# Kernel tuning notes

Measured on AMD Instinct MI355X. Metric: run time of the kernel, lower is better.

## Reference

```python
import jax, jax.numpy as jnp
import numpy as np

N = 50000      # nodes
E = 800000     # edges (avg degree 16)
D = 3          # dim_world
L = 128        # latent_dim
STEPS = 10     # message passing steps
RID = 64       # num_rigid_ids
REMB = 16      # rigid_embedding_dim


def _mlp2(x, w1, b1, w2, b2):
    # 2-layer MLP: Linear -> ReLU -> Linear (layer_norm=False, dropout=0)
    return jnp.maximum(x @ w1 + b1, 0.0) @ w2 + b2


def setup_inputs() -> dict:
    key = jax.random.key(0)
    ks = jax.random.split(key, 24)
    f32 = jnp.float32

    def lin(k, i, o):
        return (jax.random.normal(k, (i, o), f32) / np.sqrt(i)).astype(f32)

    node_in = 2 * D + 1 + REMB   # 23
    edge_in = 2 * D + 2 + 1      # 9

    receivers = jax.random.randint(ks[4], (E,), 0, N)
    # no self edges (radius_graph uses include_self_edges=False)
    senders = (receivers + jax.random.randint(ks[3], (E,), 1, N)) % N

    inp = {
        'positions': jax.random.uniform(ks[0], (N, D), f32),
        'velocities': jax.random.normal(ks[1], (N, D), f32),
        'rigid_id': jax.random.randint(ks[2], (N,), 0, RID),
        'senders': senders,
        'receivers': receivers,
        'rigid_emb': jax.random.normal(ks[5], (RID, REMB), f32) * 0.1,
        # node encoder
        'ne_w1': lin(ks[6], node_in, L), 'ne_b1': jnp.zeros((L,), f32),
        'ne_w2': lin(ks[7], L, L),       'ne_b2': jnp.zeros((L,), f32),
        # edge encoder
        'ee_w1': lin(ks[8], edge_in, L), 'ee_b1': jnp.zeros((L,), f32),
        'ee_w2': lin(ks[9], L, L),       'ee_b2': jnp.zeros((L,), f32),
        # processor blocks (stacked over STEPS)
        'pe_w1': (jax.random.normal(ks[10], (STEPS, 3 * L, L), f32) / np.sqrt(3 * L)).astype(f32),
        'pe_b1': jnp.zeros((STEPS, L), f32),
        'pe_w2': (jax.random.normal(ks[11], (STEPS, L, L), f32) / np.sqrt(L)).astype(f32),
        'pe_b2': jnp.zeros((STEPS, L), f32),
        'pn_w1': (jax.random.normal(ks[12], (STEPS, 2 * L, L), f32) / np.sqrt(2 * L)).astype(f32),
        'pn_b1': jnp.zeros((STEPS, L), f32),
        'pn_w2': (jax.random.normal(ks[13], (STEPS, L, L), f32) / np.sqrt(L)).astype(f32),
        'pn_b2': jnp.zeros((STEPS, L), f32),
        # decoder (2 layers -> output_dim = D)
        'de_w1': lin(ks[14], L, L), 'de_b1': jnp.zeros((L,), f32),
        'de_w2': lin(ks[15], L, D), 'de_b2': jnp.zeros((D,), f32),
    }
    return inp


def reference(positions, velocities, rigid_id, senders, receivers, rigid_emb,
              ne_w1, ne_b1, ne_w2, ne_b2, ee_w1, ee_b1, ee_w2, ee_b2,
              pe_w1, pe_b1, pe_w2, pe_b2, pn_w1, pn_b1, pn_w2, pn_b2,
              de_w1, de_b1, de_w2, de_b2):
    n = positions.shape[0]
    dt = positions.dtype

    # ----- feature construction (build_gns_graph_inputs + rigid features) -----
    deg = jax.ops.segment_sum(jnp.ones(receivers.shape, dt), receivers, num_segments=n)[:, None]
    center = positions.mean(axis=0, keepdims=True)
    rigid_feat = rigid_emb[rigid_id]                                # [N, REMB]
    node_feat = jnp.concatenate([velocities, positions - center, deg, rigid_feat], axis=-1)

    rel_pos = positions[senders] - positions[receivers]             # [E, D]
    rel_vel = velocities[senders] - velocities[receivers]
    sq = jnp.sum(rel_pos * rel_pos, axis=-1, keepdims=True)
    dist = jnp.sqrt(sq)
    same = (rigid_id[senders] == rigid_id[receivers]).astype(dt)[:, None]
    edge_feat = jnp.concatenate([rel_pos, rel_vel, dist, sq, same], axis=-1)

    # ----- encode -----
    nl = _mlp2(node_feat, ne_w1, ne_b1, ne_w2, ne_b2)               # [N, L]
    el = _mlp2(edge_feat, ee_w1, ee_b1, ee_w2, ee_b2)               # [E, L]

    # ----- process: gather -> edge MLP -> scatter-add -> node MLP, residual -----
    for i in range(pe_w1.shape[0]):
        edge_in = jnp.concatenate([el, nl[senders], nl[receivers]], axis=-1)  # [E, 3L]
        el = el + _mlp2(edge_in, pe_w1[i], pe_b1[i], pe_w2[i], pe_b2[i])
        agg = jax.ops.segment_sum(el, receivers, num_segments=n)              # [N, L]
        node_in = jnp.concatenate([nl, agg], axis=-1)                         # [N, 2L]
        nl = nl + _mlp2(node_in, pn_w1[i], pn_b1[i], pn_w2[i], pn_b2[i])

    # ----- decode -----
    return _mlp2(nl, de_w1, de_b1, de_w2, de_b2)                    # [N, D]
```

## Files before the change

### kernel.cpp

```cpp
#include <hip/hip_runtime.h>
#include <hip/hip_bf16.h>

#define NN 50000
#define NE 800000
#define LDIM 128
#define NSTEPS 10

typedef __hip_bfloat16 bf16;
typedef __bf16 bf8v __attribute__((ext_vector_type(8)));
typedef float f4v __attribute__((ext_vector_type(4)));
typedef unsigned short u16x8 __attribute__((ext_vector_type(8)));

__device__ inline float bflo(unsigned int u) {
    union { unsigned int i; float f; } x; x.i = u << 16; return x.f;
}
__device__ inline float bfhi(unsigned int u) {
    union { unsigned int i; float f; } x; x.i = u & 0xffff0000u; return x.f;
}
__device__ inline unsigned short f2bf(float f) {
    __hip_bfloat16 h = __float2bfloat16(f);
    unsigned short u; __builtin_memcpy(&u, &h, 2); return u;
}


__global__ void k_hist(const int* __restrict__ rcv, int* __restrict__ cnt) {
    int i = blockIdx.x * 256 + threadIdx.x;
    if (i < NE) atomicAdd(&cnt[rcv[i]], 1);
}

__global__ __launch_bounds__(1024) void k_scan(
    const int* __restrict__ cnt, int* __restrict__ row_start,
    int* __restrict__ cur, float* __restrict__ degf) {
    __shared__ int part[1024];
    const int t = threadIdx.x;
    const int CH = (NN + 1023) / 1024;
    int b0 = t * CH, b1 = b0 + CH; if (b1 > NN) b1 = NN; if (b0 > NN) b0 = NN;
    int s = 0;
    for (int i = b0; i < b1; i++) s += cnt[i];
    part[t] = s;
    __syncthreads();
    for (int off = 1; off < 1024; off <<= 1) {
        int v = (t >= off) ? part[t - off] : 0;
        __syncthreads();
        part[t] += v;
        __syncthreads();
    }
    int run = part[t] - s;
    for (int i = b0; i < b1; i++) {
        row_start[i] = run; cur[i] = run; degf[i] = (float)cnt[i];
        run += cnt[i];
    }
    if (t == 1023) row_start[NN] = part[1023];
}

__global__ void k_scatter(const int* __restrict__ snd, const int* __restrict__ rcv,
                          int* __restrict__ cur,
                          unsigned short* __restrict__ snd_p, unsigned short* __restrict__ rcv_p) {
    int i = blockIdx.x * 256 + threadIdx.x;
    if (i < NE) {
        int r = rcv[i];
        int p = atomicAdd(&cur[r], 1);
        snd_p[p] = (unsigned short)snd[i];
        rcv_p[p] = (unsigned short)r;
    }
}

__global__ void k_center(const float* __restrict__ pos, float* __restrict__ csum) {
    __shared__ float s[3][256];
    float a = 0.f, b = 0.f, c = 0.f;
    for (int i = blockIdx.x * 256 + threadIdx.x; i < NN; i += gridDim.x * 256) {
        a += pos[3 * i]; b += pos[3 * i + 1]; c += pos[3 * i + 2];
    }
    int t = threadIdx.x;
    s[0][t] = a; s[1][t] = b; s[2][t] = c;
    __syncthreads();
    for (int off = 128; off > 0; off >>= 1) {
        if (t < off) {
            s[0][t] += s[0][t + off];
            s[1][t] += s[1][t + off];
            s[2][t] += s[2][t + off];
        }
        __syncthreads();
    }
    if (t == 0) {
        atomicAdd(&csum[0], s[0][0]);
        atomicAdd(&csum[1], s[1][0]);
        atomicAdd(&csum[2], s[2][0]);
    }
}


__global__ void k_prep_w(const float* __restrict__ w, unsigned short* __restrict__ wf,
                         int KT, int Ksrc, int lo) {
    int b = blockIdx.x;
    int s = b / (KT * 8), rem = b % (KT * 8);
    int kt = rem / 8, nt = rem % 8;
    int lane = threadIdx.x, col = lane & 15, quad = lane >> 4;
    const float* W = w + (size_t)s * Ksrc * 128;
    u16x8 o;
#pragma unroll
    for (int jj = 0; jj < 8; jj++) {
        int k = kt * 32 + quad * 8 + jj;
        float x = (k < Ksrc) ? W[(size_t)k * 128 + nt * 16 + col] : 0.f;
        unsigned short h = f2bf(x);
        if (lo) h = f2bf(x - bflo(h));
        o[jj] = h;
    }
    *(u16x8*)(wf + (((size_t)b) * 64 + lane) * 8) = o;
}


__global__ __launch_bounds__(256) void k_agg(
    const unsigned short* __restrict__ el, const int* __restrict__ row_start,
    unsigned short* __restrict__ agg) {
    const int wave = threadIdx.x >> 6, lane = threadIdx.x & 63;
    const int n = blockIdx.x * 4 + wave;
    if (n >= NN) return;
    const int sub = lane >> 4, c16 = lane & 15;
    const int st = row_start[n], en = row_start[n + 1];
    float s[8];
#pragma unroll
    for (int k = 0; k < 8; k++) s[k] = 0.f;
    for (int q = st + sub; q < en; q += 4) {
        uint4 v = *(const uint4*)(el + (size_t)q * 128 + c16 * 8);
        s[0] += bflo(v.x); s[1] += bfhi(v.x);
        s[2] += bflo(v.y); s[3] += bfhi(v.y);
        s[4] += bflo(v.z); s[5] += bfhi(v.z);
        s[6] += bflo(v.w); s[7] += bfhi(v.w);
    }
#pragma unroll
    for (int k = 0; k < 8; k++) {
        s[k] += __shfl_xor(s[k], 16);
        s[k] += __shfl_xor(s[k], 32);
    }
    if (sub == 0) {
        u16x8 o;
#pragma unroll
        for (int k = 0; k < 8; k++) o[k] = f2bf(s[k]);
        *(u16x8*)(agg + (size_t)n * 128 + c16 * 8) = o;
    }
}


__global__ __launch_bounds__(256) void k_node_enc_m(
    const float* __restrict__ pos, const float* __restrict__ vel,
    const int* __restrict__ rid, const float* __restrict__ remb,
    const float* __restrict__ degf, const float* __restrict__ csum,
    const unsigned short* __restrict__ w1h, const unsigned short* __restrict__ w1l,
    const float* __restrict__ b1,
    const unsigned short* __restrict__ w2h, const unsigned short* __restrict__ w2l,
    const float* __restrict__ b2,
    unsigned short* __restrict__ nlh, unsigned short* __restrict__ nll) {
    __shared__ __align__(16) unsigned short feat_s[32 * 72];
    __shared__ __align__(16) unsigned short hid_s[32 * 264];
    const int tid = threadIdx.x, wave = tid >> 6, lane = tid & 63;
    const int col = lane & 15, quad = lane >> 4;
    bf8v W1H[2], W1L[2], W2H[4][2], W2L[4][2];
#pragma unroll
    for (int t = 0; t < 2; t++) {
        W1H[t] = *(const bf8v*)(w1h + ((size_t)(2 * wave + t) * 64 + lane) * 8);
        W1L[t] = *(const bf8v*)(w1l + ((size_t)(2 * wave + t) * 64 + lane) * 8);
    }
#pragma unroll
    for (int kt = 0; kt < 4; kt++)
#pragma unroll
        for (int t = 0; t < 2; t++) {
            W2H[kt][t] = *(const bf8v*)(w2h + ((size_t)(kt * 8 + 2 * wave + t) * 64 + lane) * 8);
            W2L[kt][t] = *(const bf8v*)(w2l + ((size_t)(kt * 8 + 2 * wave + t) * 64 + lane) * 8);
        }
    float bias1[2], bias2[2];
#pragma unroll
    for (int t = 0; t < 2; t++) {
        bias1[t] = b1[(2 * wave + t) * 16 + col];
        bias2[t] = b2[(2 * wave + t) * 16 + col];
    }
    float cx = csum[0] * (1.0f / NN), cy = csum[1] * (1.0f / NN), cz = csum[2] * (1.0f / NN);
    uint4 z = {0u, 0u, 0u, 0u};
    for (int s2 = tid; s2 < 288; s2 += 256) *(uint4*)(feat_s + s2 * 8) = z;

    for (int it = 0; it < 4; it++) {
        const int base = blockIdx.x * 128 + it * 32;
        if (base >= NN) break;
        __syncthreads();
        if (tid < 32) {
            int n = base + tid; if (n > NN - 1) n = NN - 1;
            float v[23];
            v[0] = vel[3 * n]; v[1] = vel[3 * n + 1]; v[2] = vel[3 * n + 2];
            v[3] = pos[3 * n] - cx; v[4] = pos[3 * n + 1] - cy; v[5] = pos[3 * n + 2] - cz;
            v[6] = degf[n];
            int rb = rid[n] * 16;
#pragma unroll
            for (int k = 0; k < 16; k++) v[7 + k] = remb[rb + k];
            unsigned short* f = feat_s + tid * 72;
#pragma unroll
            for (int k = 0; k < 23; k++) {
                unsigned short h = f2bf(v[k]);
                f[k] = h; f[32 + k] = f2bf(v[k] - bflo(h));
            }
        }
        __syncthreads();
        f4v acc[2][2];
#pragma unroll
        for (int mt = 0; mt < 2; mt++)
#pragma unroll
            for (int t = 0; t < 2; t++) acc[mt][t] = (f4v){0.f, 0.f, 0.f, 0.f};
        {
            bf8v a0h = *(const bf8v*)(feat_s + col * 72 + quad * 8);
            bf8v a1h = *(const bf8v*)(feat_s + (16 + col) * 72 + quad * 8);
            bf8v a0l = *(const bf8v*)(feat_s + col * 72 + 32 + quad * 8);
            bf8v a1l = *(const bf8v*)(feat_s + (16 + col) * 72 + 32 + quad * 8);
#pragma unroll
            for (int t = 0; t < 2; t++) {
                acc[0][t] = __builtin_amdgcn_mfma_f32_16x16x32_bf16(a0h, W1H[t], acc[0][t], 0, 0, 0);
                acc[1][t] = __builtin_amdgcn_mfma_f32_16x16x32_bf16(a1h, W1H[t], acc[1][t], 0, 0, 0);
                acc[0][t] = __builtin_amdgcn_mfma_f32_16x16x32_bf16(a0l, W1H[t], acc[0][t], 0, 0, 0);
                acc[1][t] = __builtin_amdgcn_mfma_f32_16x16x32_bf16(a1l, W1H[t], acc[1][t], 0, 0, 0);
                acc[0][t] = __builtin_amdgcn_mfma_f32_16x16x32_bf16(a0h, W1L[t], acc[0][t], 0, 0, 0);
                acc[1][t] = __builtin_amdgcn_mfma_f32_16x16x32_bf16(a1h, W1L[t], acc[1][t], 0, 0, 0);
            }
        }
#pragma unroll
        for (int mt = 0; mt < 2; mt++)
#pragma unroll
            for (int t = 0; t < 2; t++) {
                const int nc = (2 * wave + t) * 16 + col;
#pragma unroll
                for (int r = 0; r < 4; r++) {
                    float h = fmaxf(acc[mt][t][r] + bias1[t], 0.f);
                    unsigned short hh = f2bf(h);
                    hid_s[(mt * 16 + quad * 4 + r) * 264 + nc] = hh;
                    hid_s[(mt * 16 + quad * 4 + r) * 264 + 128 + nc] = f2bf(h - bflo(hh));
                }
            }
        __syncthreads();
#pragma unroll
        for (int mt = 0; mt < 2; mt++)
#pragma unroll
            for (int t = 0; t < 2; t++) acc[mt][t] = (f4v){0.f, 0.f, 0.f, 0.f};
#pragma unroll
        for (int kt = 0; kt < 8; kt++) {
            int w = kt & 3;
            bf8v a0 = *(const bf8v*)(hid_s + col * 264 + kt * 32 + quad * 8);
            bf8v a1 = *(const bf8v*)(hid_s + (16 + col) * 264 + kt * 32 + quad * 8);
#pragma unroll
            for (int t = 0; t < 2; t++) {
                acc[0][t] = __builtin_amdgcn_mfma_f32_16x16x32_bf16(a0, W2H[w][t], acc[0][t], 0, 0, 0);
                acc[1][t] = __builtin_amdgcn_mfma_f32_16x16x32_bf16(a1, W2H[w][t], acc[1][t], 0, 0, 0);
            }
        }
#pragma unroll
        for (int kt = 0; kt < 4; kt++) {
            bf8v a0 = *(const bf8v*)(hid_s + col * 264 + kt * 32 + quad * 8);
            bf8v a1 = *(const bf8v*)(hid_s + (16 + col) * 264 + kt * 32 + quad * 8);
#pragma unroll
            for (int t = 0; t < 2; t++) {
                acc[0][t] = __builtin_amdgcn_mfma_f32_16x16x32_bf16(a0, W2L[kt][t], acc[0][t], 0, 0, 0);
                acc[1][t] = __builtin_amdgcn_mfma_f32_16x16x32_bf16(a1, W2L[kt][t], acc[1][t], 0, 0, 0);
            }
        }
        __syncthreads();
#pragma unroll
        for (int mt = 0; mt < 2; mt++)
#pragma unroll
            for (int t = 0; t < 2; t++) {
                const int nc = (2 * wave + t) * 16 + col;
#pragma unroll
                for (int r = 0; r < 4; r++) {
                    const int row = mt * 16 + quad * 4 + r;
                    float v = acc[mt][t][r] + bias2[t];
                    unsigned short hh = f2bf(v);
                    hid_s[row * 264 + nc] = hh;
                    hid_s[row * 264 + 128 + nc] = f2bf(v - bflo(hh));
                }
            }
        __syncthreads();
#pragma unroll
        for (int p = 0; p < 2; p++) {
            int s2 = p * 256 + tid, e = s2 >> 4, c16 = s2 & 15;
            if (base + e < NN) {
                *(uint4*)(nlh + (size_t)(base + e) * 128 + c16 * 8) =
                    *(const uint4*)(hid_s + e * 264 + c16 * 8);
                *(uint4*)(nll + (size_t)(base + e) * 128 + c16 * 8) =
                    *(const uint4*)(hid_s + e * 264 + 128 + c16 * 8);
            }
        }
    }
}


__global__ __launch_bounds__(256) void k_edge_enc_m(
    const float* __restrict__ pos, const float* __restrict__ vel,
    const int* __restrict__ rid,
    const unsigned short* __restrict__ snd, const unsigned short* __restrict__ rcv,
    const unsigned short* __restrict__ w1h, const unsigned short* __restrict__ w1l,
    const float* __restrict__ b1,
    const unsigned short* __restrict__ w2h, const unsigned short* __restrict__ w2l,
    const float* __restrict__ b2,
    unsigned short* __restrict__ el) {
    __shared__ __align__(16) unsigned short feat_s[32 * 72];
    __shared__ __align__(16) unsigned short hid_s[32 * 264];
    const int tid = threadIdx.x, wave = tid >> 6, lane = tid & 63;
    const int col = lane & 15, quad = lane >> 4;
    bf8v W1H[2], W1L[2], W2H[4][2], W2L[4][2];
#pragma unroll
    for (int t = 0; t < 2; t++) {
        W1H[t] = *(const bf8v*)(w1h + ((size_t)(2 * wave + t) * 64 + lane) * 8);
        W1L[t] = *(const bf8v*)(w1l + ((size_t)(2 * wave + t) * 64 + lane) * 8);
    }
#pragma unroll
    for (int kt = 0; kt < 4; kt++)
#pragma unroll
        for (int t = 0; t < 2; t++) {
            W2H[kt][t] = *(const bf8v*)(w2h + ((size_t)(kt * 8 + 2 * wave + t) * 64 + lane) * 8);
            W2L[kt][t] = *(const bf8v*)(w2l + ((size_t)(kt * 8 + 2 * wave + t) * 64 + lane) * 8);
        }
    float bias1[2], bias2[2];
#pragma unroll
    for (int t = 0; t < 2; t++) {
        bias1[t] = b1[(2 * wave + t) * 16 + col];
        bias2[t] = b2[(2 * wave + t) * 16 + col];
    }
    uint4 z = {0u, 0u, 0u, 0u};
    for (int s2 = tid; s2 < 288; s2 += 256) *(uint4*)(feat_s + s2 * 8) = z;

    for (int it = 0; it < 4; it++) {
        const int base = blockIdx.x * 128 + it * 32;
        __syncthreads();
        if (tid < 32) {
            int e = base + tid;
            int s = snd[e], r = rcv[e];
            float v[9];
            v[0] = pos[3 * s] - pos[3 * r]; v[1] = pos[3 * s + 1] - pos[3 * r + 1]; v[2] = pos[3 * s + 2] - pos[3 * r + 2];
            v[3] = vel[3 * s] - vel[3 * r]; v[4] = vel[3 * s + 1] - vel[3 * r + 1]; v[5] = vel[3 * s + 2] - vel[3 * r + 2];
            float sq = v[0] * v[0] + v[1] * v[1] + v[2] * v[2];
            v[6] = sqrtf(sq); v[7] = sq;
            v[8] = (rid[s] == rid[r]) ? 1.f : 0.f;
            unsigned short* f = feat_s + tid * 72;
#pragma unroll
            for (int k = 0; k < 9; k++) {
                unsigned short h = f2bf(v[k]);
                f[k] = h; f[32 + k] = f2bf(v[k] - bflo(h));
            }
        }
        __syncthreads();
        f4v acc[2][2];
#pragma unroll
        for (int mt = 0; mt < 2; mt++)
#pragma unroll
            for (int t = 0; t < 2; t++) acc[mt][t] = (f4v){0.f, 0.f, 0.f, 0.f};
        {
            bf8v a0h = *(const bf8v*)(feat_s + col * 72 + quad * 8);
            bf8v a1h = *(const bf8v*)(feat_s + (16 + col) * 72 + quad * 8);
            bf8v a0l = *(const bf8v*)(feat_s + col * 72 + 32 + quad * 8);
            bf8v a1l = *(const bf8v*)(feat_s + (16 + col) * 72 + 32 + quad * 8);
#pragma unroll
            for (int t = 0; t < 2; t++) {
                acc[0][t] = __builtin_amdgcn_mfma_f32_16x16x32_bf16(a0h, W1H[t], acc[0][t], 0, 0, 0);
                acc[1][t] = __builtin_amdgcn_mfma_f32_16x16x32_bf16(a1h, W1H[t], acc[1][t], 0, 0, 0);
                acc[0][t] = __builtin_amdgcn_mfma_f32_16x16x32_bf16(a0l, W1H[t], acc[0][t], 0, 0, 0);
                acc[1][t] = __builtin_amdgcn_mfma_f32_16x16x32_bf16(a1l, W1H[t], acc[1][t], 0, 0, 0);
                acc[0][t] = __builtin_amdgcn_mfma_f32_16x16x32_bf16(a0h, W1L[t], acc[0][t], 0, 0, 0);
                acc[1][t] = __builtin_amdgcn_mfma_f32_16x16x32_bf16(a1h, W1L[t], acc[1][t], 0, 0, 0);
            }
        }
#pragma unroll
        for (int mt = 0; mt < 2; mt++)
#pragma unroll
            for (int t = 0; t < 2; t++) {
                const int nc = (2 * wave + t) * 16 + col;
#pragma unroll
                for (int r = 0; r < 4; r++) {
                    float h = fmaxf(acc[mt][t][r] + bias1[t], 0.f);
                    unsigned short hh = f2bf(h);
                    hid_s[(mt * 16 + quad * 4 + r) * 264 + nc] = hh;
                    hid_s[(mt * 16 + quad * 4 + r) * 264 + 128 + nc] = f2bf(h - bflo(hh));
                }
            }
        __syncthreads();
#pragma unroll
        for (int mt = 0; mt < 2; mt++)
#pragma unroll
            for (int t = 0; t < 2; t++) acc[mt][t] = (f4v){0.f, 0.f, 0.f, 0.f};
#pragma unroll
        for (int kt = 0; kt < 8; kt++) {
            int w = kt & 3;
            bf8v a0 = *(const bf8v*)(hid_s + col * 264 + kt * 32 + quad * 8);
            bf8v a1 = *(const bf8v*)(hid_s + (16 + col) * 264 + kt * 32 + quad * 8);
#pragma unroll
            for (int t = 0; t < 2; t++) {
                acc[0][t] = __builtin_amdgcn_mfma_f32_16x16x32_bf16(a0, W2H[w][t], acc[0][t], 0, 0, 0);
                acc[1][t] = __builtin_amdgcn_mfma_f32_16x16x32_bf16(a1, W2H[w][t], acc[1][t], 0, 0, 0);
            }
        }
#pragma unroll
        for (int kt = 0; kt < 4; kt++) {
            bf8v a0 = *(const bf8v*)(hid_s + col * 264 + kt * 32 + quad * 8);
            bf8v a1 = *(const bf8v*)(hid_s + (16 + col) * 264 + kt * 32 + quad * 8);
#pragma unroll
            for (int t = 0; t < 2; t++) {
                acc[0][t] = __builtin_amdgcn_mfma_f32_16x16x32_bf16(a0, W2L[kt][t], acc[0][t], 0, 0, 0);
                acc[1][t] = __builtin_amdgcn_mfma_f32_16x16x32_bf16(a1, W2L[kt][t], acc[1][t], 0, 0, 0);
            }
        }
        __syncthreads();
#pragma unroll
        for (int mt = 0; mt < 2; mt++)
#pragma unroll
            for (int t = 0; t < 2; t++) {
                const int nc = (2 * wave + t) * 16 + col;
#pragma unroll
                for (int r = 0; r < 4; r++)
                    hid_s[(mt * 16 + quad * 4 + r) * 264 + nc] = f2bf(acc[mt][t][r] + bias2[t]);
            }
        __syncthreads();
#pragma unroll
        for (int p = 0; p < 2; p++) {
            int s2 = p * 256 + tid, e = s2 >> 4, c16 = s2 & 15;
            *(uint4*)(el + (size_t)(base + e) * 128 + c16 * 8) =
                *(const uint4*)(hid_s + e * 264 + c16 * 8);
        }
    }
}


__global__ __launch_bounds__(256) void k_edge_step(
    unsigned short* __restrict__ el, const unsigned short* __restrict__ nlh,
    const unsigned short* __restrict__ snd, const unsigned short* __restrict__ rcv,
    const unsigned short* __restrict__ w1f, const float* __restrict__ b1,
    const unsigned short* __restrict__ w2f, const float* __restrict__ b2) {
    __shared__ __align__(16) unsigned short inl_s[32 * 392];
    __shared__ __align__(16) unsigned short hid_s[32 * 136];
    const int tid = threadIdx.x;
    const int wave = tid >> 6, lane = tid & 63;
    const int col = lane & 15, quad = lane >> 4;
    const int erow = tid >> 4, c16 = tid & 15;

    bf8v W1[12][2], W2[4][2];
#pragma unroll
    for (int kt = 0; kt < 12; kt++)
#pragma unroll
        for (int t = 0; t < 2; t++)
            W1[kt][t] = *(const bf8v*)(w1f + ((size_t)(kt * 8 + 2 * wave + t) * 64 + lane) * 8);
#pragma unroll
    for (int kt = 0; kt < 4; kt++)
#pragma unroll
        for (int t = 0; t < 2; t++)
            W2[kt][t] = *(const bf8v*)(w2f + ((size_t)(kt * 8 + 2 * wave + t) * 64 + lane) * 8);
    float bias1[2], bias2[2];
#pragma unroll
    for (int t = 0; t < 2; t++) {
        bias1[t] = b1[(2 * wave + t) * 16 + col];
        bias2[t] = b2[(2 * wave + t) * 16 + col];
    }

    uint4 pf_s[2];
#pragma unroll
    for (int p = 0; p < 2; p++) {
        int ge = blockIdx.x * 128 + p * 16 + erow;
        pf_s[p] = *(const uint4*)(nlh + (size_t)snd[ge] * 128 + c16 * 8);
    }

    for (int it = 0; it < 4; it++) {
        const int base = blockIdx.x * 128 + it * 32;
        __syncthreads();
#pragma unroll
        for (int p = 0; p < 2; p++) {
            int e = p * 16 + erow;
            int ge = base + e;
            *(uint4*)(inl_s + e * 392 + c16 * 8) =
                *(const uint4*)(el + (size_t)ge * 128 + c16 * 8);
            *(uint4*)(inl_s + e * 392 + 128 + c16 * 8) = pf_s[p];
            *(uint4*)(inl_s + e * 392 + 256 + c16 * 8) =
                *(const uint4*)(nlh + (size_t)rcv[ge] * 128 + c16 * 8);
        }
        if (it < 3) {
#pragma unroll
            for (int p = 0; p < 2; p++) {
                int ge = base + 32 + p * 16 + erow;
                pf_s[p] = *(const uint4*)(nlh + (size_t)snd[ge] * 128 + c16 * 8);
            }
        }
        __syncthreads();

        f4v acc[2][2];
#pragma unroll
        for (int mt = 0; mt < 2; mt++)
#pragma unroll
            for (int t = 0; t < 2; t++) acc[mt][t] = (f4v){0.f, 0.f, 0.f, 0.f};
#pragma unroll
        for (int kt = 0; kt < 12; kt++) {
            bf8v a0 = *(const bf8v*)(inl_s + col * 392 + kt * 32 + quad * 8);
            bf8v a1 = *(const bf8v*)(inl_s + (16 + col) * 392 + kt * 32 + quad * 8);
            acc[0][0] = __builtin_amdgcn_mfma_f32_16x16x32_bf16(a0, W1[kt][0], acc[0][0], 0, 0, 0);
            acc[0][1] = __builtin_amdgcn_mfma_f32_16x16x32_bf16(a0, W1[kt][1], acc[0][1], 0, 0, 0);
            acc[1][0] = __builtin_amdgcn_mfma_f32_16x16x32_bf16(a1, W1[kt][0], acc[1][0], 0, 0, 0);
            acc[1][1] = __builtin_amdgcn_mfma_f32_16x16x32_bf16(a1, W1[kt][1], acc[1][1], 0, 0, 0);
        }
#pragma unroll
        for (int mt = 0; mt < 2; mt++)
#pragma unroll
            for (int t = 0; t < 2; t++) {
                const int nc = (2 * wave + t) * 16 + col;
#pragma unroll
                for (int r = 0; r < 4; r++) {
                    float v = fmaxf(acc[mt][t][r] + bias1[t], 0.f);
                    hid_s[(mt * 16 + quad * 4 + r) * 136 + nc] = f2bf(v);
                }
            }
        __syncthreads();

#pragma unroll
        for (int mt = 0; mt < 2; mt++)
#pragma unroll
            for (int t = 0; t < 2; t++) acc[mt][t] = (f4v){0.f, 0.f, 0.f, 0.f};
#pragma unroll
        for (int kt = 0; kt < 4; kt++) {
            bf8v a0 = *(const bf8v*)(hid_s + col * 136 + kt * 32 + quad * 8);
            bf8v a1 = *(const bf8v*)(hid_s + (16 + col) * 136 + kt * 32 + quad * 8);
            acc[0][0] = __builtin_amdgcn_mfma_f32_16x16x32_bf16(a0, W2[kt][0], acc[0][0], 0, 0, 0);
            acc[0][1] = __builtin_amdgcn_mfma_f32_16x16x32_bf16(a0, W2[kt][1], acc[0][1], 0, 0, 0);
            acc[1][0] = __builtin_amdgcn_mfma_f32_16x16x32_bf16(a1, W2[kt][0], acc[1][0], 0, 0, 0);
            acc[1][1] = __builtin_amdgcn_mfma_f32_16x16x32_bf16(a1, W2[kt][1], acc[1][1], 0, 0, 0);
        }
        __syncthreads();
#pragma unroll
        for (int mt = 0; mt < 2; mt++)
#pragma unroll
            for (int t = 0; t < 2; t++) {
                const int nc = (2 * wave + t) * 16 + col;
#pragma unroll
                for (int r = 0; r < 4; r++) {
                    const int row = mt * 16 + quad * 4 + r;
                    float v = acc[mt][t][r] + bias2[t] + bflo((unsigned int)inl_s[row * 392 + nc]);
                    hid_s[row * 136 + nc] = f2bf(v);
                }
            }
        __syncthreads();
#pragma unroll
        for (int p = 0; p < 2; p++) {
            int e = p * 16 + erow;
            *(uint4*)(el + (size_t)(base + e) * 128 + c16 * 8) =
                *(const uint4*)(hid_s + e * 136 + c16 * 8);
        }
    }
}


__global__ __launch_bounds__(256) void k_node_step_s(
    unsigned short* __restrict__ nlh, unsigned short* __restrict__ nll,
    const unsigned short* __restrict__ agg,
    const unsigned short* __restrict__ w1h, const unsigned short* __restrict__ w1l,
    const float* __restrict__ b1,
    const unsigned short* __restrict__ w2h, const unsigned short* __restrict__ w2l,
    const float* __restrict__ b2) {
    __shared__ __align__(16) unsigned short a_s[32 * 392];
    __shared__ __align__(16) unsigned short hid_s[32 * 264];
    const int tid = threadIdx.x, wave = tid >> 6, lane = tid & 63;
    const int col = lane & 15, quad = lane >> 4;
    bf8v W1H[8][2], W1L[8][2], W2H[4][2], W2L[4][2];
#pragma unroll
    for (int kt = 0; kt < 8; kt++)
#pragma unroll
        for (int t = 0; t < 2; t++) {
            W1H[kt][t] = *(const bf8v*)(w1h + ((size_t)(kt * 8 + 2 * wave + t) * 64 + lane) * 8);
            W1L[kt][t] = *(const bf8v*)(w1l + ((size_t)(kt * 8 + 2 * wave + t) * 64 + lane) * 8);
        }
#pragma unroll
    for (int kt = 0; kt < 4; kt++)
#pragma unroll
        for (int t = 0; t < 2; t++) {
            W2H[kt][t] = *(const bf8v*)(w2h + ((size_t)(kt * 8 + 2 * wave + t) * 64 + lane) * 8);
            W2L[kt][t] = *(const bf8v*)(w2l + ((size_t)(kt * 8 + 2 * wave + t) * 64 + lane) * 8);
        }
    float bias1[2], bias2[2];
#pragma unroll
    for (int t = 0; t < 2; t++) {
        bias1[t] = b1[(2 * wave + t) * 16 + col];
        bias2[t] = b2[(2 * wave + t) * 16 + col];
    }
    for (int it = 0; it < 2; it++) {
        const int base = blockIdx.x * 64 + it * 32;
        if (base >= NN) break;
        __syncthreads();
#pragma unroll
        for (int p = 0; p < 2; p++) {
            int e = p * 16 + (tid >> 4), c16 = tid & 15;
            int n = base + e; if (n > NN - 1) n = NN - 1;
            *(uint4*)(a_s + e * 392 + c16 * 8) =
                *(const uint4*)(nlh + (size_t)n * 128 + c16 * 8);
            *(uint4*)(a_s + e * 392 + 128 + c16 * 8) =
                *(const uint4*)(nll + (size_t)n * 128 + c16 * 8);
            *(uint4*)(a_s + e * 392 + 256 + c16 * 8) =
                *(const uint4*)(agg + (size_t)n * 128 + c16 * 8);
        }
        __syncthreads();

        f4v acc[2][2];
#pragma unroll
        for (int mt = 0; mt < 2; mt++)
#pragma unroll
            for (int t = 0; t < 2; t++) acc[mt][t] = (f4v){0.f, 0.f, 0.f, 0.f};
#pragma unroll
        for (int kt = 0; kt < 8; kt++) {
            bf8v a0 = *(const bf8v*)(a_s + col * 392 + kt * 32 + quad * 8);
            bf8v a1 = *(const bf8v*)(a_s + (16 + col) * 392 + kt * 32 + quad * 8);
#pragma unroll
            for (int t = 0; t < 2; t++) {
                acc[0][t] = __builtin_amdgcn_mfma_f32_16x16x32_bf16(a0, W1H[kt & 3][t], acc[0][t], 0, 0, 0);
                acc[1][t] = __builtin_amdgcn_mfma_f32_16x16x32_bf16(a1, W1H[kt & 3][t], acc[1][t], 0, 0, 0);
            }
        }
#pragma unroll
        for (int kt = 0; kt < 4; kt++) {
            bf8v a0 = *(const bf8v*)(a_s + col * 392 + 256 + kt * 32 + quad * 8);
            bf8v a1 = *(const bf8v*)(a_s + (16 + col) * 392 + 256 + kt * 32 + quad * 8);
#pragma unroll
            for (int t = 0; t < 2; t++) {
                acc[0][t] = __builtin_amdgcn_mfma_f32_16x16x32_bf16(a0, W1H[4 + kt][t], acc[0][t], 0, 0, 0);
                acc[1][t] = __builtin_amdgcn_mfma_f32_16x16x32_bf16(a1, W1H[4 + kt][t], acc[1][t], 0, 0, 0);
            }
        }
#pragma unroll
        for (int kt = 0; kt < 4; kt++) {
            bf8v a0 = *(const bf8v*)(a_s + col * 392 + kt * 32 + quad * 8);
            bf8v a1 = *(const bf8v*)(a_s + (16 + col) * 392 + kt * 32 + quad * 8);
#pragma unroll
            for (int t = 0; t < 2; t++) {
                acc[0][t] = __builtin_amdgcn_mfma_f32_16x16x32_bf16(a0, W1L[kt][t], acc[0][t], 0, 0, 0);
                acc[1][t] = __builtin_amdgcn_mfma_f32_16x16x32_bf16(a1, W1L[kt][t], acc[1][t], 0, 0, 0);
            }
        }
#pragma unroll
        for (int kt = 0; kt < 4; kt++) {
            bf8v a0 = *(const bf8v*)(a_s + col * 392 + 256 + kt * 32 + quad * 8);
            bf8v a1 = *(const bf8v*)(a_s + (16 + col) * 392 + 256 + kt * 32 + quad * 8);
#pragma unroll
            for (int t = 0; t < 2; t++) {
                acc[0][t] = __builtin_amdgcn_mfma_f32_16x16x32_bf16(a0, W1L[4 + kt][t], acc[0][t], 0, 0, 0);
                acc[1][t] = __builtin_amdgcn_mfma_f32_16x16x32_bf16(a1, W1L[4 + kt][t], acc[1][t], 0, 0, 0);
            }
        }
#pragma unroll
        for (int mt = 0; mt < 2; mt++)
#pragma unroll
            for (int t = 0; t < 2; t++) {
                const int nc = (2 * wave + t) * 16 + col;
#pragma unroll
                for (int r = 0; r < 4; r++) {
                    float h = fmaxf(acc[mt][t][r] + bias1[t], 0.f);
                    unsigned short hh = f2bf(h);
                    hid_s[(mt * 16 + quad * 4 + r) * 264 + nc] = hh;
                    hid_s[(mt * 16 + quad * 4 + r) * 264 + 128 + nc] = f2bf(h - bflo(hh));
                }
            }
        __syncthreads();
#pragma unroll
        for (int mt = 0; mt < 2; mt++)
#pragma unroll
            for (int t = 0; t < 2; t++) acc[mt][t] = (f4v){0.f, 0.f, 0.f, 0.f};
#pragma unroll
        for (int kt = 0; kt < 8; kt++) {
            int w = kt & 3;
            bf8v a0 = *(const bf8v*)(hid_s + col * 264 + kt * 32 + quad * 8);
            bf8v a1 = *(const bf8v*)(hid_s + (16 + col) * 264 + kt * 32 + quad * 8);
#pragma unroll
            for (int t = 0; t < 2; t++) {
                acc[0][t] = __builtin_amdgcn_mfma_f32_16x16x32_bf16(a0, W2H[w][t], acc[0][t], 0, 0, 0);
                acc[1][t] = __builtin_amdgcn_mfma_f32_16x16x32_bf16(a1, W2H[w][t], acc[1][t], 0, 0, 0);
            }
        }
#pragma unroll
        for (int kt = 0; kt < 4; kt++) {
            bf8v a0 = *(const bf8v*)(hid_s + col * 264 + kt * 32 + quad * 8);
            bf8v a1 = *(const bf8v*)(hid_s + (16 + col) * 264 + kt * 32 + quad * 8);
#pragma unroll
            for (int t = 0; t < 2; t++) {
                acc[0][t] = __builtin_amdgcn_mfma_f32_16x16x32_bf16(a0, W2L[kt][t], acc[0][t], 0, 0, 0);
                acc[1][t] = __builtin_amdgcn_mfma_f32_16x16x32_bf16(a1, W2L[kt][t], acc[1][t], 0, 0, 0);
            }
        }
        __syncthreads();
#pragma unroll
        for (int mt = 0; mt < 2; mt++)
#pragma unroll
            for (int t = 0; t < 2; t++) {
                const int nc = (2 * wave + t) * 16 + col;
#pragma unroll
                for (int r = 0; r < 4; r++) {
                    const int row = mt * 16 + quad * 4 + r;
                    float res = bflo((unsigned int)a_s[row * 392 + nc]) +
                                bflo((unsigned int)a_s[row * 392 + 128 + nc]);
                    float v = acc[mt][t][r] + bias2[t] + res;
                    unsigned short hh = f2bf(v);
                    hid_s[row * 264 + nc] = hh;
                    hid_s[row * 264 + 128 + nc] = f2bf(v - bflo(hh));
                }
            }
        __syncthreads();
#pragma unroll
        for (int p = 0; p < 2; p++) {
            int e = p * 16 + (tid >> 4), c16 = tid & 15;
            if (base + e < NN) {
                *(uint4*)(nlh + (size_t)(base + e) * 128 + c16 * 8) =
                    *(const uint4*)(hid_s + e * 264 + c16 * 8);
                *(uint4*)(nll + (size_t)(base + e) * 128 + c16 * 8) =
                    *(const uint4*)(hid_s + e * 264 + 128 + c16 * 8);
            }
        }
    }
}


__global__ __launch_bounds__(128) void k_decode(
    const unsigned short* __restrict__ nlh, const unsigned short* __restrict__ nll,
    const float* __restrict__ w1, const float* __restrict__ b1,
    const float* __restrict__ w2, const float* __restrict__ b2,
    float* __restrict__ out) {
    __shared__ float inl[16][128];
    __shared__ float hid[16][128];
    int j = threadIdx.x;
    int base = blockIdx.x * 16;
    for (int e = 0; e < 16; e++)
        inl[e][j] = bflo((unsigned int)nlh[(size_t)(base + e) * 128 + j]) +
                    bflo((unsigned int)nll[(size_t)(base + e) * 128 + j]);
    __syncthreads();
    float acc[16];
#pragma unroll
    for (int e = 0; e < 16; e++) acc[e] = b1[j];
    for (int kc = 0; kc < 16; kc++) {
        float w[8];
#pragma unroll
        for (int t = 0; t < 8; t++) w[t] = w1[(kc * 8 + t) * 128 + j];
#pragma unroll
        for (int e = 0; e < 16; e++) {
            float4 h0 = *(const float4*)&inl[e][kc * 8];
            float4 h1 = *(const float4*)&inl[e][kc * 8 + 4];
            acc[e] = fmaf(h0.x, w[0], acc[e]); acc[e] = fmaf(h0.y, w[1], acc[e]);
            acc[e] = fmaf(h0.z, w[2], acc[e]); acc[e] = fmaf(h0.w, w[3], acc[e]);
            acc[e] = fmaf(h1.x, w[4], acc[e]); acc[e] = fmaf(h1.y, w[5], acc[e]);
            acc[e] = fmaf(h1.z, w[6], acc[e]); acc[e] = fmaf(h1.w, w[7], acc[e]);
        }
    }
#pragma unroll
    for (int e = 0; e < 16; e++) hid[e][j] = fmaxf(acc[e], 0.f);
    __syncthreads();
    if (j < 48) {
        int e = j / 3, ch = j - 3 * (j / 3);
        float s = b2[ch];
        for (int k = 0; k < 128; k++) s = fmaf(hid[e][k], w2[k * 3 + ch], s);
        out[(size_t)(base + e) * 3 + ch] = s;
    }
}


extern "C" void kernel_launch(void* const* d_in, const int* in_sizes, int n_in,
                              void* d_out, int out_size, void* d_ws, size_t ws_size,
                              hipStream_t stream) {
    (void)in_sizes; (void)n_in; (void)out_size; (void)ws_size;
    const float* pos   = (const float*)d_in[0];
    const float* vel   = (const float*)d_in[1];
    const int*   rid   = (const int*)d_in[2];
    const int*   snd   = (const int*)d_in[3];
    const int*   rcv   = (const int*)d_in[4];
    const float* remb  = (const float*)d_in[5];
    const float* ne_w1 = (const float*)d_in[6];
    const float* ne_b1 = (const float*)d_in[7];
    const float* ne_w2 = (const float*)d_in[8];
    const float* ne_b2 = (const float*)d_in[9];
    const float* ee_w1 = (const float*)d_in[10];
    const float* ee_b1 = (const float*)d_in[11];
    const float* ee_w2 = (const float*)d_in[12];
    const float* ee_b2 = (const float*)d_in[13];
    const float* pe_w1 = (const float*)d_in[14];
    const float* pe_b1 = (const float*)d_in[15];
    const float* pe_w2 = (const float*)d_in[16];
    const float* pe_b2 = (const float*)d_in[17];
    const float* pn_w1 = (const float*)d_in[18];
    const float* pn_b1 = (const float*)d_in[19];
    const float* pn_w2 = (const float*)d_in[20];
    const float* pn_b2 = (const float*)d_in[21];
    const float* de_w1 = (const float*)d_in[22];
    const float* de_b1 = (const float*)d_in[23];
    const float* de_w2 = (const float*)d_in[24];
    const float* de_b2 = (const float*)d_in[25];
    float* out = (float*)d_out;

    char* p = (char*)d_ws;
    auto carve = [&](size_t bytes) { void* q = (void*)p; p += (bytes + 15) & ~(size_t)15; return q; };
    unsigned short* el    = (unsigned short*)carve((size_t)NE * LDIM * 2);
    unsigned short* nlh   = (unsigned short*)carve((size_t)NN * LDIM * 2);
    unsigned short* nll   = (unsigned short*)carve((size_t)NN * LDIM * 2);
    unsigned short* agg   = (unsigned short*)carve((size_t)NN * LDIM * 2);
    unsigned short* w1f_e = (unsigned short*)carve((size_t)NSTEPS * 12 * 8 * 512 * 2);
    unsigned short* w2f_e = (unsigned short*)carve((size_t)NSTEPS * 4 * 8 * 512 * 2);
    unsigned short* w1h_n = (unsigned short*)carve((size_t)NSTEPS * 8 * 8 * 512 * 2);
    unsigned short* w1l_n = (unsigned short*)carve((size_t)NSTEPS * 8 * 8 * 512 * 2);
    unsigned short* w2h_n = (unsigned short*)carve((size_t)NSTEPS * 4 * 8 * 512 * 2);
    unsigned short* w2l_n = (unsigned short*)carve((size_t)NSTEPS * 4 * 8 * 512 * 2);
    unsigned short* eew1h = (unsigned short*)carve((size_t)1 * 8 * 512 * 2);
    unsigned short* eew1l = (unsigned short*)carve((size_t)1 * 8 * 512 * 2);
    unsigned short* eew2h = (unsigned short*)carve((size_t)4 * 8 * 512 * 2);
    unsigned short* eew2l = (unsigned short*)carve((size_t)4 * 8 * 512 * 2);
    unsigned short* new1h = (unsigned short*)carve((size_t)1 * 8 * 512 * 2);
    unsigned short* new1l = (unsigned short*)carve((size_t)1 * 8 * 512 * 2);
    unsigned short* new2h = (unsigned short*)carve((size_t)4 * 8 * 512 * 2);
    unsigned short* new2l = (unsigned short*)carve((size_t)4 * 8 * 512 * 2);
    unsigned short* snd_p = (unsigned short*)carve((size_t)NE * 2);
    unsigned short* rcv_p = (unsigned short*)carve((size_t)NE * 2);
    int*            rs    = (int*)carve((size_t)(NN + 1) * 4);
    int*            cnt   = (int*)carve((size_t)NN * 4);
    int*            cur   = (int*)carve((size_t)NN * 4);
    float*          degf  = (float*)carve((size_t)NN * 4);
    float*          csum  = (float*)carve(16);

    hipMemsetAsync(cnt, 0, (size_t)NN * 4, stream);
    hipMemsetAsync(csum, 0, 16, stream);
    k_hist<<<NE / 256, 256, 0, stream>>>(rcv, cnt);
    k_scan<<<1, 1024, 0, stream>>>(cnt, rs, cur, degf);
    k_center<<<64, 256, 0, stream>>>(pos, csum);
    k_scatter<<<NE / 256, 256, 0, stream>>>(snd, rcv, cur, snd_p, rcv_p);
    k_prep_w<<<NSTEPS * 12 * 8, 64, 0, stream>>>(pe_w1, w1f_e, 12, 384, 0);
    k_prep_w<<<NSTEPS * 4 * 8, 64, 0, stream>>>(pe_w2, w2f_e, 4, 128, 0);
    k_prep_w<<<NSTEPS * 8 * 8, 64, 0, stream>>>(pn_w1, w1h_n, 8, 256, 0);
    k_prep_w<<<NSTEPS * 8 * 8, 64, 0, stream>>>(pn_w1, w1l_n, 8, 256, 1);
    k_prep_w<<<NSTEPS * 4 * 8, 64, 0, stream>>>(pn_w2, w2h_n, 4, 128, 0);
    k_prep_w<<<NSTEPS * 4 * 8, 64, 0, stream>>>(pn_w2, w2l_n, 4, 128, 1);
    k_prep_w<<<8, 64, 0, stream>>>(ee_w1, eew1h, 1, 9, 0);
    k_prep_w<<<8, 64, 0, stream>>>(ee_w1, eew1l, 1, 9, 1);
    k_prep_w<<<4 * 8, 64, 0, stream>>>(ee_w2, eew2h, 4, 128, 0);
    k_prep_w<<<4 * 8, 64, 0, stream>>>(ee_w2, eew2l, 4, 128, 1);
    k_prep_w<<<8, 64, 0, stream>>>(ne_w1, new1h, 1, 23, 0);
    k_prep_w<<<8, 64, 0, stream>>>(ne_w1, new1l, 1, 23, 1);
    k_prep_w<<<4 * 8, 64, 0, stream>>>(ne_w2, new2h, 4, 128, 0);
    k_prep_w<<<4 * 8, 64, 0, stream>>>(ne_w2, new2l, 4, 128, 1);

    k_node_enc_m<<<(NN + 127) / 128, 256, 0, stream>>>(pos, vel, rid, remb, degf, csum,
                                                       new1h, new1l, ne_b1, new2h, new2l, ne_b2, nlh, nll);
    k_edge_enc_m<<<NE / 128, 256, 0, stream>>>(pos, vel, rid, snd_p, rcv_p,
                                               eew1h, eew1l, ee_b1, eew2h, eew2l, ee_b2, el);
    for (int i = 0; i < NSTEPS; i++) {
        k_edge_step<<<NE / 128, 256, 0, stream>>>(el, nlh, snd_p, rcv_p,
            w1f_e + (size_t)i * 12 * 8 * 512, pe_b1 + i * 128,
            w2f_e + (size_t)i * 4 * 8 * 512, pe_b2 + i * 128);
        k_agg<<<(NN + 3) / 4, 256, 0, stream>>>(el, rs, agg);
        k_node_step_s<<<(NN + 63) / 64, 256, 0, stream>>>(nlh, nll, agg,
            w1h_n + (size_t)i * 8 * 8 * 512, w1l_n + (size_t)i * 8 * 8 * 512, pn_b1 + i * 128,
            w2h_n + (size_t)i * 4 * 8 * 512, w2l_n + (size_t)i * 4 * 8 * 512, pn_b2 + i * 128);
    }
    k_decode<<<NN / 16, 128, 0, stream>>>(nlh, nll, de_w1, de_b1, de_w2, de_b2, out);
}
```

Baseline: 2.895 ms.

## Fuse segment-sum into edge step via bf16 packed atomics and prefetch all gathers

Removes the separate CSR aggregation kernel and instead accumulates updated edge latents into the node aggregate from inside the edge-step kernel. It reduces runs of equal receivers (edges appear receiver-sorted) per wave and issues global_atomic_pk_add_bf16. The agg buffer is zeroed with a memset each step. The edge latent and receiver gathers are also prefetched one tile ahead, like the sender gather. This saves re-reading the whole edge tensor per step, but adds atomic contention and accumulates in bf16 through atomics, which is less precise and non-deterministic.

New measurement: 3.847 ms. 1.33x slower.

```diff
diff --git a/kernel.cpp b/kernel.cpp
--- a/kernel.cpp
+++ b/kernel.cpp
@@ -107,38 +107,6 @@
         o[jj] = h;
     }
     *(u16x8*)(wf + (((size_t)b) * 64 + lane) * 8) = o;
-}
-
-
-__global__ __launch_bounds__(256) void k_agg(
-    const unsigned short* __restrict__ el, const int* __restrict__ row_start,
-    unsigned short* __restrict__ agg) {
-    const int wave = threadIdx.x >> 6, lane = threadIdx.x & 63;
-    const int n = blockIdx.x * 4 + wave;
-    if (n >= NN) return;
-    const int sub = lane >> 4, c16 = lane & 15;
-    const int st = row_start[n], en = row_start[n + 1];
-    float s[8];
-#pragma unroll
-    for (int k = 0; k < 8; k++) s[k] = 0.f;
-    for (int q = st + sub; q < en; q += 4) {
-        uint4 v = *(const uint4*)(el + (size_t)q * 128 + c16 * 8);
-        s[0] += bflo(v.x); s[1] += bfhi(v.x);
-        s[2] += bflo(v.y); s[3] += bfhi(v.y);
-        s[4] += bflo(v.z); s[5] += bfhi(v.z);
-        s[6] += bflo(v.w); s[7] += bfhi(v.w);
-    }
-#pragma unroll
-    for (int k = 0; k < 8; k++) {
-        s[k] += __shfl_xor(s[k], 16);
-        s[k] += __shfl_xor(s[k], 32);
-    }
-    if (sub == 0) {
-        u16x8 o;
-#pragma unroll
-        for (int k = 0; k < 8; k++) o[k] = f2bf(s[k]);
-        *(u16x8*)(agg + (size_t)n * 128 + c16 * 8) = o;
-    }
 }
 
 
@@ -427,9 +395,11 @@
     unsigned short* __restrict__ el, const unsigned short* __restrict__ nlh,
     const unsigned short* __restrict__ snd, const unsigned short* __restrict__ rcv,
     const unsigned short* __restrict__ w1f, const float* __restrict__ b1,
-    const unsigned short* __restrict__ w2f, const float* __restrict__ b2) {
+    const unsigned short* __restrict__ w2f, const float* __restrict__ b2,
+    unsigned short* __restrict__ agg) {
     __shared__ __align__(16) unsigned short inl_s[32 * 392];
     __shared__ __align__(16) unsigned short hid_s[32 * 136];
+    __shared__ int rcv_s[32];
     const int tid = threadIdx.x;
     const int wave = tid >> 6, lane = tid & 63;
     const int col = lane & 15, quad = lane >> 4;
@@ -453,11 +423,13 @@
         bias2[t] = b2[(2 * wave + t) * 16 + col];
     }
 
-    uint4 pf_s[2];
+    uint4 pf_e[2], pf_s[2], pf_r[2];
 #pragma unroll
     for (int p = 0; p < 2; p++) {
         int ge = blockIdx.x * 128 + p * 16 + erow;
+        pf_e[p] = *(const uint4*)(el + (size_t)ge * 128 + c16 * 8);
         pf_s[p] = *(const uint4*)(nlh + (size_t)snd[ge] * 128 + c16 * 8);
+        pf_r[p] = *(const uint4*)(nlh + (size_t)rcv[ge] * 128 + c16 * 8);
     }
 
     for (int it = 0; it < 4; it++) {
@@ -466,18 +438,18 @@
 #pragma unroll
         for (int p = 0; p < 2; p++) {
             int e = p * 16 + erow;
-            int ge = base + e;
-            *(uint4*)(inl_s + e * 392 + c16 * 8) =
-                *(const uint4*)(el + (size_t)ge * 128 + c16 * 8);
+            *(uint4*)(inl_s + e * 392 + c16 * 8) = pf_e[p];
             *(uint4*)(inl_s + e * 392 + 128 + c16 * 8) = pf_s[p];
-            *(uint4*)(inl_s + e * 392 + 256 + c16 * 8) =
-                *(const uint4*)(nlh + (size_t)rcv[ge] * 128 + c16 * 8);
-        }
+            *(uint4*)(inl_s + e * 392 + 256 + c16 * 8) = pf_r[p];
+        }
+        if (tid < 32) rcv_s[tid] = rcv[base + tid];
         if (it < 3) {
 #pragma unroll
             for (int p = 0; p < 2; p++) {
                 int ge = base + 32 + p * 16 + erow;
+                pf_e[p] = *(const uint4*)(el + (size_t)ge * 128 + c16 * 8);
                 pf_s[p] = *(const uint4*)(nlh + (size_t)snd[ge] * 128 + c16 * 8);
+                pf_r[p] = *(const uint4*)(nlh + (size_t)rcv[ge] * 128 + c16 * 8);
             }
         }
         __syncthreads();
@@ -522,7 +494,6 @@
             acc[1][0] = __builtin_amdgcn_mfma_f32_16x16x32_bf16(a1, W2[kt][0], acc[1][0], 0, 0, 0);
             acc[1][1] = __builtin_amdgcn_mfma_f32_16x16x32_bf16(a1, W2[kt][1], acc[1][1], 0, 0, 0);
         }
-        __syncthreads();
 #pragma unroll
         for (int mt = 0; mt < 2; mt++)
 #pragma unroll
@@ -531,18 +502,55 @@
 #pragma unroll
                 for (int r = 0; r < 4; r++) {
                     const int row = mt * 16 + quad * 4 + r;
-                    float v = acc[mt][t][r] + bias2[t] + bflo((unsigned int)inl_s[row * 392 + nc]);
-                    hid_s[row * 136 + nc] = f2bf(v);
+                    float* fp = (float*)(inl_s + row * 392 + 128);
+                    fp[nc] = acc[mt][t][r] + bias2[t];
                 }
             }
         __syncthreads();
+
 #pragma unroll
         for (int p = 0; p < 2; p++) {
             int e = p * 16 + erow;
-            *(uint4*)(el + (size_t)(base + e) * 128 + c16 * 8) =
-                *(const uint4*)(hid_s + e * 136 + c16 * 8);
-        }
-    }
+            const float* fp = (const float*)(inl_s + e * 392 + 128);
+            f4v a = *(const f4v*)(fp + c16 * 8);
+            f4v b = *(const f4v*)(fp + c16 * 8 + 4);
+            uint4 rsd = *(const uint4*)(inl_s + e * 392 + c16 * 8);
+            float o0 = a[0] + bflo(rsd.x), o1 = a[1] + bfhi(rsd.x);
+            float o2 = a[2] + bflo(rsd.y), o3 = a[3] + bfhi(rsd.y);
+            float o4 = b[0] + bflo(rsd.z), o5 = b[1] + bfhi(rsd.z);
+            float o6 = b[2] + bflo(rsd.w), o7 = b[3] + bfhi(rsd.w);
+            uint4 o;
+            o.x = ((unsigned int)f2bf(o1) << 16) | f2bf(o0);
+            o.y = ((unsigned int)f2bf(o3) << 16) | f2bf(o2);
+            o.z = ((unsigned int)f2bf(o5) << 16) | f2bf(o4);
+            o.w = ((unsigned int)f2bf(o7) << 16) | f2bf(o6);
+            *(uint4*)(el + (size_t)(base + e) * 128 + c16 * 8) = o;
+        }
+
+        {
+            float r0 = 0.f, r1 = 0.f;
+            int curn = rcv_s[wave * 8];
+#pragma unroll
+            for (int e2 = wave * 8; e2 < wave * 8 + 8; ++e2) {
+                int nd = rcv_s[e2];
+                if (nd != curn) {
+                    unsigned int d = ((unsigned int)f2bf(r1) << 16) | (unsigned int)f2bf(r0);
+                    unsigned short* pa = agg + (size_t)curn * 128 + lane * 2;
+                    asm volatile("global_atomic_pk_add_bf16 %0, %1, off" :: "v"(pa), "v"(d) : "memory");
+                    r0 = r1 = 0.f; curn = nd;
+                }
+                const float* fp = (const float*)(inl_s + e2 * 392 + 128);
+                float2 v = *(const float2*)(fp + lane * 2);
+                unsigned int rr = *((const unsigned int*)(inl_s + e2 * 392) + lane);
+                r0 += v.x + bflo(rr);
+                r1 += v.y + bfhi(rr);
+            }
+            unsigned int d = ((unsigned int)f2bf(r1) << 16) | (unsigned int)f2bf(r0);
+            unsigned short* pa = agg + (size_t)curn * 128 + lane * 2;
+            asm volatile("global_atomic_pk_add_bf16 %0, %1, off" :: "v"(pa), "v"(d) : "memory");
+        }
+    }
+    asm volatile("s_waitcnt vmcnt(0)" ::: "memory");
 }
 
 
@@ -839,10 +847,10 @@
     k_edge_enc_m<<<NE / 128, 256, 0, stream>>>(pos, vel, rid, snd_p, rcv_p,
                                                eew1h, eew1l, ee_b1, eew2h, eew2l, ee_b2, el);
     for (int i = 0; i < NSTEPS; i++) {
+        hipMemsetAsync(agg, 0, (size_t)NN * LDIM * 2, stream);
         k_edge_step<<<NE / 128, 256, 0, stream>>>(el, nlh, snd_p, rcv_p,
             w1f_e + (size_t)i * 12 * 8 * 512, pe_b1 + i * 128,
-            w2f_e + (size_t)i * 4 * 8 * 512, pe_b2 + i * 128);
-        k_agg<<<(NN + 3) / 4, 256, 0, stream>>>(el, rs, agg);
+            w2f_e + (size_t)i * 4 * 8 * 512, pe_b2 + i * 128, agg);
         k_node_step_s<<<(NN + 63) / 64, 256, 0, stream>>>(nlh, nll, agg,
             w1h_n + (size_t)i * 8 * 8 * 512, w1l_n + (size_t)i * 8 * 8 * 512, pn_b1 + i * 128,
             w2h_n + (size_t)i * 4 * 8 * 512, w2l_n + (size_t)i * 4 * 8 * 512, pn_b2 + i * 128);
```

## Double-buffer edge-step gathers with async global-to-LDS loads and XOR swizzle

Applied to the files above, without the earlier changes.

The edge step kernel now gathers edge latents and sender/receiver node rows straight into LDS with global_load_lds DMA. It uses two stage buffers so the next 32-edge tile loads while the current tile runs its MFMAs, replacing the register-staged copy and its extra barrier. The copy order is XOR-swizzled per row so the unpadded 256-byte rows can be read without LDS bank conflicts, and the residual read uses the same swizzle. The risk is correctness if the async LDS writes are not properly waited on before the barrier. It also uses more LDS, which may lower occupancy.

After: 2.889 ms (median of 2 runs). About the same (-0.2%).

```diff
diff --git a/kernel.cpp b/kernel.cpp
--- a/kernel.cpp
+++ b/kernel.cpp
@@ -20,6 +20,12 @@
 __device__ inline unsigned short f2bf(float f) {
     __hip_bfloat16 h = __float2bfloat16(f);
     unsigned short u; __builtin_memcpy(&u, &h, 2); return u;
+}
+
+__device__ __forceinline__ void gl_lds16(const void* g, void* l) {
+    __builtin_amdgcn_global_load_lds(
+        (const __attribute__((address_space(1))) unsigned int*)g,
+        (__attribute__((address_space(3))) unsigned int*)l, 16, 0, 0);
 }
 
 
@@ -428,7 +434,7 @@
     const unsigned short* __restrict__ snd, const unsigned short* __restrict__ rcv,
     const unsigned short* __restrict__ w1f, const float* __restrict__ b1,
     const unsigned short* __restrict__ w2f, const float* __restrict__ b2) {
-    __shared__ __align__(16) unsigned short inl_s[32 * 392];
+    __shared__ __align__(1024) unsigned short stage_s[2][3][32][128];
     __shared__ __align__(16) unsigned short hid_s[32 * 136];
     const int tid = threadIdx.x;
     const int wave = tid >> 6, lane = tid & 63;
@@ -453,44 +459,61 @@
         bias2[t] = b2[(2 * wave + t) * 16 + col];
     }
 
-    uint4 pf_s[2];
-#pragma unroll
-    for (int p = 0; p < 2; p++) {
-        int ge = blockIdx.x * 128 + p * 16 + erow;
-        pf_s[p] = *(const uint4*)(nlh + (size_t)snd[ge] * 128 + c16 * 8);
-    }
+    const int srow0 = wave * 8 + (lane >> 4);
+    const int srow1 = srow0 + 4;
+    const int skb = (lane & 15) * 16;
+    const int soff0 = skb ^ ((srow0 & 7) << 4);
+    const int soff1 = skb ^ ((srow1 & 7) << 4);
+    const int gb0 = blockIdx.x * 128;
+    const char* elc = (const char*)el;
+    const char* nlc = (const char*)nlh;
+
+    auto issue = [&](int t, int b, int si0, int si1, int ri0, int ri1) {
+        char* s0 = (char*)&stage_s[b][0][wave * 8][0];
+        char* s1 = (char*)&stage_s[b][1][wave * 8][0];
+        char* s2 = (char*)&stage_s[b][2][wave * 8][0];
+        const size_t gb = (size_t)(gb0 + t * 32);
+        gl_lds16(elc + (gb + srow0) * 256 + soff0, s0);
+        gl_lds16(elc + (gb + srow1) * 256 + soff1, s0 + 1024);
+        gl_lds16(nlc + (size_t)si0 * 256 + soff0, s1);
+        gl_lds16(nlc + (size_t)si1 * 256 + soff1, s1 + 1024);
+        gl_lds16(nlc + (size_t)ri0 * 256 + soff0, s2);
+        gl_lds16(nlc + (size_t)ri1 * 256 + soff1, s2 + 1024);
+    };
+
+    {
+        int si0 = snd[gb0 + srow0], si1 = snd[gb0 + srow1];
+        int ri0 = rcv[gb0 + srow0], ri1 = rcv[gb0 + srow1];
+        issue(0, 0, si0, si1, ri0, ri1);
+    }
+    int nsi0 = snd[gb0 + 32 + srow0], nsi1 = snd[gb0 + 32 + srow1];
+    int nri0 = rcv[gb0 + 32 + srow0], nri1 = rcv[gb0 + 32 + srow1];
 
     for (int it = 0; it < 4; it++) {
-        const int base = blockIdx.x * 128 + it * 32;
-        __syncthreads();
-#pragma unroll
-        for (int p = 0; p < 2; p++) {
-            int e = p * 16 + erow;
-            int ge = base + e;
-            *(uint4*)(inl_s + e * 392 + c16 * 8) =
-                *(const uint4*)(el + (size_t)ge * 128 + c16 * 8);
-            *(uint4*)(inl_s + e * 392 + 128 + c16 * 8) = pf_s[p];
-            *(uint4*)(inl_s + e * 392 + 256 + c16 * 8) =
-                *(const uint4*)(nlh + (size_t)rcv[ge] * 128 + c16 * 8);
-        }
+        const int cur = it & 1, nxt = cur ^ 1;
+        const int base = gb0 + it * 32;
+        __syncthreads();
         if (it < 3) {
-#pragma unroll
-            for (int p = 0; p < 2; p++) {
-                int ge = base + 32 + p * 16 + erow;
-                pf_s[p] = *(const uint4*)(nlh + (size_t)snd[ge] * 128 + c16 * 8);
-            }
-        }
-        __syncthreads();
+            issue(it + 1, nxt, nsi0, nsi1, nri0, nri1);
+            if (it < 2) {
+                int gb = gb0 + (it + 2) * 32;
+                nsi0 = snd[gb + srow0]; nsi1 = snd[gb + srow1];
+                nri0 = rcv[gb + srow0]; nri1 = rcv[gb + srow1];
+            }
+        }
 
         f4v acc[2][2];
 #pragma unroll
         for (int mt = 0; mt < 2; mt++)
 #pragma unroll
             for (int t = 0; t < 2; t++) acc[mt][t] = (f4v){0.f, 0.f, 0.f, 0.f};
+        const int sw = (col & 7) << 4;
 #pragma unroll
         for (int kt = 0; kt < 12; kt++) {
-            bf8v a0 = *(const bf8v*)(inl_s + col * 392 + kt * 32 + quad * 8);
-            bf8v a1 = *(const bf8v*)(inl_s + (16 + col) * 392 + kt * 32 + quad * 8);
+            const char* sb = (const char*)&stage_s[cur][kt >> 2][0][0];
+            const int kb = (kt & 3) * 64 + quad * 16;
+            bf8v a0 = *(const bf8v*)(sb + col * 256 + (kb ^ sw));
+            bf8v a1 = *(const bf8v*)(sb + (16 + col) * 256 + (kb ^ sw));
             acc[0][0] = __builtin_amdgcn_mfma_f32_16x16x32_bf16(a0, W1[kt][0], acc[0][0], 0, 0, 0);
             acc[0][1] = __builtin_amdgcn_mfma_f32_16x16x32_bf16(a0, W1[kt][1], acc[0][1], 0, 0, 0);
             acc[1][0] = __builtin_amdgcn_mfma_f32_16x16x32_bf16(a1, W1[kt][0], acc[1][0], 0, 0, 0);
@@ -523,6 +546,7 @@
             acc[1][1] = __builtin_amdgcn_mfma_f32_16x16x32_bf16(a1, W2[kt][1], acc[1][1], 0, 0, 0);
         }
         __syncthreads();
+
 #pragma unroll
         for (int mt = 0; mt < 2; mt++)
 #pragma unroll
@@ -531,7 +555,8 @@
 #pragma unroll
                 for (int r = 0; r < 4; r++) {
                     const int row = mt * 16 + quad * 4 + r;
-                    float v = acc[mt][t][r] + bias2[t] + bflo((unsigned int)inl_s[row * 392 + nc]);
+                    float res = bflo((unsigned int)stage_s[cur][0][row][nc ^ ((row & 7) << 3)]);
+                    float v = acc[mt][t][r] + bias2[t] + res;
                     hid_s[row * 136 + nc] = f2bf(v);
                 }
             }
```
